# Performance work log

Hardware: AMD Instinct MI355X
Metric: run time of the kernel (lower is better)

Reference implementation:

```python
import jax, jax.numpy as jnp
import numpy as np

D = 1024
H = 8
HD = D // H
SCALE = HD ** -0.5


def setup_inputs() -> dict:
    key = jax.random.key(0)
    ks = jax.random.split(key, 12)
    s = 0.02
    return {
        "x": jax.random.normal(ks[0], (4, 2048, D), dtype=jnp.float32),
        "attn_mask": jax.random.randint(ks[1], (2048, 2048), 0, 2, dtype=jnp.int32),
        "qkv_w": jax.random.normal(ks[2], (3 * D, D), dtype=jnp.float32) * s,
        "qkv_b": jnp.zeros((3 * D,), dtype=jnp.float32),
        "q_w": jax.random.normal(ks[3], (D, D), dtype=jnp.float32) * s,
        "q_b": jnp.zeros((D,), dtype=jnp.float32),
        "k_w": jax.random.normal(ks[4], (D, D), dtype=jnp.float32) * s,
        "k_b": jnp.zeros((D,), dtype=jnp.float32),
        "v_w": jax.random.normal(ks[5], (D, D), dtype=jnp.float32) * s,
        "v_b": jnp.zeros((D,), dtype=jnp.float32),
        "out_w": jax.random.normal(ks[6], (D, D), dtype=jnp.float32) * s,
        "out_b": jnp.zeros((D,), dtype=jnp.float32),
    }


def reference(x, attn_mask, qkv_w, qkv_b, q_w, q_b, k_w, k_b, v_w, v_b, out_w, out_b):
    B, S, _ = x.shape
    qkv = x @ qkv_w.T + qkv_b
    q, k, v = jnp.split(qkv, 3, axis=-1)
    # per-stream multi-head projections, then split heads: [B,H,S,HD]
    def heads(t, w, b):
        return (t @ w.T + b).reshape(B, S, H, HD).transpose(0, 2, 1, 3)
    q = heads(q, q_w, q_b)
    k = heads(k, k_w, k_b)
    v = heads(v, v_w, v_b)
    # scaled dot-product attention with masked softmax
    scores = jnp.einsum("bhqd,bhkd->bhqk", q, k) * SCALE
    scores = jnp.where(attn_mask == 1, -jnp.inf, scores)
    attn = jax.nn.softmax(scores, axis=-1)
    o = jnp.einsum("bhqk,bhkd->bhqd", attn, v)
    o = o.transpose(0, 2, 1, 3).reshape(B, S, D)
    return o @ out_w.T + out_b
```

## Files before the change

### kernel.cpp

```cpp
#include <hip/hip_runtime.h>
#include <stdint.h>

typedef unsigned short u16;
typedef unsigned int u32;
typedef unsigned long long u64;
using f32x4 = __attribute__((ext_vector_type(4))) float;
using f32x16 = __attribute__((ext_vector_type(16))) float;
using s16x8 = __attribute__((ext_vector_type(8))) short;
using u16x4 = __attribute__((ext_vector_type(4))) unsigned short;
using u32x4 = __attribute__((ext_vector_type(4))) u32;

static constexpr float kQScale = (float)(0.08838834764831845 * 1.4426950408889634);

__device__ __forceinline__ u16 f2bf(float f) {
  uint32_t u = __float_as_uint(f);
  u += 0x7fffu + ((u >> 16) & 1u);
  return (u16)(u >> 16);
}

__device__ __forceinline__ float fexp2(float x) {
#if __has_builtin(__builtin_amdgcn_exp2f)
  return __builtin_amdgcn_exp2f(x);
#else
  return exp2f(x);
#endif
}

__device__ __forceinline__ u32 cvtpk(float lo, float hi) {
  u32 r;
  asm("v_cvt_pk_bf16_f32 %0, %1, %2" : "=v"(r) : "v"(lo), "v"(hi));
  return r;
}

__device__ __forceinline__ void mfma16(f32x4& d, s16x8 a, s16x8 b) {
  asm volatile("v_mfma_f32_16x16x32_bf16 %0, %1, %2, %0" : "+v"(d) : "v"(a), "v"(b));
}
__device__ __forceinline__ void mfma32(f32x16& d, s16x8 a, s16x8 b) {
  asm volatile("v_mfma_f32_32x32x16_bf16 %0, %1, %2, %0" : "+v"(d) : "v"(a), "v"(b));
}
__device__ __forceinline__ f32x16 mfma32_z(s16x8 a, s16x8 b) {
  f32x16 d;
  asm volatile("v_mfma_f32_32x32x16_bf16 %0, %1, %2, 0" : "=&v"(d) : "v"(a), "v"(b));
  return d;
}

__device__ __forceinline__ void g2lds16(const void* g, void* l) {
  __builtin_amdgcn_global_load_lds(
      (__attribute__((address_space(1))) void*)(uintptr_t)g,
      (__attribute__((address_space(3))) void*)(uint32_t)(uintptr_t)l, 16, 0, 0);
}

#define BAR() asm volatile("s_barrier" ::: "memory")

__global__ __launch_bounds__(256) void cvt_f32_bf16(const float* __restrict__ in,
                                                    u16* __restrict__ out, int n) {
  int i = (blockIdx.x * 256 + threadIdx.x) * 4;
  if (i + 3 < n) {
    f32x4 v = *(const f32x4*)(in + i);
    u16x4 o = {f2bf(v.x), f2bf(v.y), f2bf(v.z), f2bf(v.w)};
    *(u16x4*)(out + i) = o;
  }
}

__global__ __launch_bounds__(256) void cvt4(const float* __restrict__ a, const float* __restrict__ b,
                                            const float* __restrict__ c, const float* __restrict__ d,
                                            u16* __restrict__ out) {
  int z = blockIdx.y;
  const float* in = z == 0 ? a : z == 1 ? b : z == 2 ? c : d;
  int i = (blockIdx.x * 256 + threadIdx.x) * 4;
  f32x4 v = *(const f32x4*)(in + i);
  u16x4 o = {f2bf(v.x), f2bf(v.y), f2bf(v.z), f2bf(v.w)};
  *(u16x4*)(out + (size_t)z * 1048576 + i) = o;
}

__global__ __launch_bounds__(256) void transpose_f32_bf16(const float* __restrict__ in,
                                                          u16* __restrict__ out, int R, int C) {
  __shared__ u16 tile[32][33];
  int bx = blockIdx.x, by = blockIdx.y;
  int tx = threadIdx.x & 31, ty = threadIdx.x >> 5;
#pragma unroll
  for (int k = 0; k < 4; ++k)
    tile[ty + k * 8][tx] = f2bf(in[(size_t)(by * 32 + ty + k * 8) * C + bx * 32 + tx]);
  __syncthreads();
#pragma unroll
  for (int k = 0; k < 4; ++k)
    out[(size_t)(bx * 32 + ty + k * 8) * R + by * 32 + tx] = tile[tx][ty + k * 8];
}

__global__ __launch_bounds__(256) void cbias3(const float* __restrict__ qw, const float* __restrict__ kw,
                                              const float* __restrict__ vw, const float* __restrict__ qkvb,
                                              const float* __restrict__ qb, const float* __restrict__ kb,
                                              const float* __restrict__ vb, float* __restrict__ out) {
  int z = blockIdx.y;
  const float* w = z == 0 ? qw : (z == 1 ? kw : vw);
  const float* ba = z == 0 ? qb : (z == 1 ? kb : vb);
  const float* bi = qkvb + z * 1024;
  int o = blockIdx.x * 4 + (threadIdx.x >> 6);
  int lane = threadIdx.x & 63;
  float s = 0.f;
  for (int m = lane; m < 1024; m += 64) s += w[o * 1024 + m] * bi[m];
#pragma unroll
  for (int d = 1; d < 64; d <<= 1) s += __shfl_xor(s, d);
  if (lane == 0) {
    float fin = s + ba[o];
    if (z == 0) fin *= kQScale;
    out[z * 1024 + o] = fin;
  }
}

__global__ __launch_bounds__(256) void pack_mask(const int* __restrict__ m, u64* __restrict__ pm) {
  int row = blockIdx.x;
  int wv = threadIdx.x >> 6, lane = threadIdx.x & 63;
#pragma unroll
  for (int i = 0; i < 8; ++i) {
    int word = wv * 8 + i;
    u64 b = __ballot(m[(size_t)row * 2048 + word * 64 + lane] == 0);
    if (lane == 0) pm[(size_t)row * 32 + word] = b;
  }
}

template <typename OUT_T, bool BIAS_PER_ROW>
__global__ __launch_bounds__(256, 2) void gemm_nt(const u16* __restrict__ A, int lda, long bsA,
                                                  const u16* __restrict__ B, int ldb, long bsB,
                                                  OUT_T* __restrict__ C, int ldc, long bsC,
                                                  const float* __restrict__ bias, long bsBias,
                                                  int NtilesN, int K, float scale_z0) {
  __shared__ __align__(16) u16 As[128 * 64];
  __shared__ __align__(16) u16 Bs[128 * 64];
  const int z = blockIdx.z;
  const float sc = (z == 0) ? scale_z0 : 1.f;
  A += (size_t)z * bsA; B += (size_t)z * bsB; C += (size_t)z * bsC;
  if (bias) bias += (size_t)z * bsBias;
  const int tm = blockIdx.x / NtilesN, tn = blockIdx.x % NtilesN;
  const int tid = threadIdx.x, lane = tid & 63, w = tid >> 6;
  const int wm = w >> 1, wn = w & 1;
  const int q = lane & 15, g = lane >> 4;
  f32x4 acc[4][4] = {};

  const u16* Ab = A + (size_t)(tm * 128 + (tid >> 3)) * lda + ((tid & 7) << 3);
  const u16* Bb = B + (size_t)(tn * 128 + (tid >> 3)) * ldb + ((tid & 7) << 3);
  char* AsW = (char*)As + (w << 10);
  char* BsW = (char*)Bs + (w << 10);

  for (int k0 = 0; k0 < K; k0 += 64) {
#pragma unroll
    for (int it = 0; it < 4; ++it) {
      g2lds16(Ab + (size_t)(it * 32) * lda + k0, AsW + it * 4096);
      g2lds16(Bb + (size_t)(it * 32) * ldb + k0, BsW + it * 4096);
    }
    __syncthreads();
#pragma unroll
    for (int kk = 0; kk < 2; ++kk) {
      s16x8 af[4], bf[4];
#pragma unroll
      for (int i = 0; i < 4; ++i)
        af[i] = *(const s16x8*)((const char*)As + (wm * 64 + i * 16 + q) * 128 + kk * 64 + g * 16);
#pragma unroll
      for (int i = 0; i < 4; ++i)
        bf[i] = *(const s16x8*)((const char*)Bs + (wn * 64 + i * 16 + q) * 128 + kk * 64 + g * 16);
#pragma unroll
      for (int mf = 0; mf < 4; ++mf)
#pragma unroll
        for (int nf = 0; nf < 4; ++nf) mfma16(acc[mf][nf], af[mf], bf[nf]);
    }
    __syncthreads();
  }
  asm volatile("s_nop 7\n\ts_nop 7");
#pragma unroll
  for (int mf = 0; mf < 4; ++mf)
#pragma unroll
    for (int nf = 0; nf < 4; ++nf) {
      const int row = tm * 128 + wm * 64 + mf * 16 + g * 4;
      const int col = tn * 128 + wn * 64 + nf * 16 + q;
      float bc = (!BIAS_PER_ROW && bias) ? bias[col] : 0.f;
#pragma unroll
      for (int r = 0; r < 4; ++r) {
        float v = acc[mf][nf][r] * sc;
        if (bias) v += BIAS_PER_ROW ? bias[row + r] : bc;
        if constexpr (sizeof(OUT_T) == 2)
          C[(size_t)(row + r) * ldc + col] = (OUT_T)f2bf(v);
        else
          C[(size_t)(row + r) * ldc + col] = (OUT_T)v;
      }
    }
}

__global__ __launch_bounds__(512, 1) void gemm256(const u16* __restrict__ A, int lda,
                                                  const u16* __restrict__ B, int ldb,
                                                  u16* __restrict__ C, int ldc,
                                                  const float* __restrict__ bias,
                                                  int K, int NtN) {
  __shared__ __align__(16) u16 Als[2][256 * 64];
  __shared__ __align__(16) u16 Bls[2][256 * 64];
  const int bid = blockIdx.x;
  const int cpx = gridDim.x >> 3;
  const int wgid = (bid & 7) * cpx + (bid >> 3);
  const int tm = wgid / NtN, tn = wgid % NtN;
  const int tid = threadIdx.x, lane = tid & 63, w = tid >> 6;
  const int wm = w >> 2, wn = w & 3;
  const int q = lane & 15, g = lane >> 4, qk = q & 7;
  const int nT = K >> 6;

  f32x4 acc[8][4] = {};
  s16x8 af[4][2], bf[4][2];

  const int srow = tid >> 3, sch = tid & 7;
  const int gcol = (sch ^ (srow & 7)) << 3;
  const u16* Abase = A + (size_t)(tm * 256 + srow) * lda + gcol;
  const u16* Bbase = B + (size_t)(tn * 256 + srow) * ldb + gcol;

  auto stageA = [&](int buf, int kt, int h) {
    const u16* s0 = Abase + (size_t)(h * 128) * lda + (kt << 6);
    char* d = (char*)&Als[buf][0] + h * 16384 + (w << 10);
    g2lds16(s0, d);
    g2lds16(s0 + (size_t)64 * lda, d + 8192);
  };
  auto stageB = [&](int buf, int kt, int h) {
    const u16* s0 = Bbase + (size_t)(h * 128) * ldb + (kt << 6);
    char* d = (char*)&Bls[buf][0] + h * 16384 + (w << 10);
    g2lds16(s0, d);
    g2lds16(s0 + (size_t)64 * ldb, d + 8192);
  };
  auto loadA = [&](const char* base, int mh) {
#pragma unroll
    for (int mf = 0; mf < 4; ++mf)
#pragma unroll
      for (int kk = 0; kk < 2; ++kk)
        af[mf][kk] = *(const s16x8*)(base + (mh * 128 + wm * 64 + mf * 16 + q) * 128 +
                                     ((((kk << 2) + g) ^ qk) << 4));
  };
  auto loadB = [&](const char* base, int nh) {
#pragma unroll
    for (int nf = 0; nf < 2; ++nf)
#pragma unroll
      for (int kk = 0; kk < 2; ++kk)
        bf[nh * 2 + nf][kk] = *(const s16x8*)(base + (nh * 128 + wn * 32 + nf * 16 + q) * 128 +
                                              ((((kk << 2) + g) ^ qk) << 4));
  };
  auto quad = [&](int mh, int nh) {
    __builtin_amdgcn_s_setprio(1);
#pragma unroll
    for (int mf = 0; mf < 4; ++mf)
#pragma unroll
      for (int nf = 0; nf < 2; ++nf)
#pragma unroll
        for (int kk = 0; kk < 2; ++kk)
          mfma16(acc[mh * 4 + mf][nh * 2 + nf], af[mf][kk], bf[nh * 2 + nf][kk]);
    __builtin_amdgcn_s_setprio(0);
  };

  stageA(0, 0, 0); stageA(0, 0, 1); stageB(0, 0, 0); stageB(0, 0, 1);
  const int kt1 = (1 < nT) ? 1 : 0;
  stageB(1, kt1, 0); stageB(1, kt1, 1);
  asm volatile("s_waitcnt vmcnt(4)" ::: "memory");
  BAR();

  for (int kt = 0; kt < nT; ++kt) {
    const int buf = kt & 1;
    const char* Ab = (const char*)&Als[buf][0];
    const char* Bb = (const char*)&Bls[buf][0];
    const int ktA = (kt + 1 < nT) ? kt + 1 : nT - 1;
    const int ktB = (kt + 2 < nT) ? kt + 2 : nT - 1;
    loadA(Ab, 0); loadB(Bb, 0);
    stageA(buf ^ 1, ktA, 0);
    BAR();
    quad(0, 0);
    BAR();
    loadB(Bb, 1);
    stageA(buf ^ 1, ktA, 1);
    BAR();
    quad(0, 1);
    asm volatile("s_waitcnt vmcnt(8)" ::: "memory");
    BAR();
    loadA(Ab, 1);
    stageB(buf, ktB, 0);
    BAR();
    quad(1, 0);
    BAR();
    stageB(buf, ktB, 1);
    BAR();
    quad(1, 1);
    asm volatile("s_waitcnt vmcnt(6)" ::: "memory");
    BAR();
  }

  asm volatile("s_nop 7\n\ts_nop 7");
#pragma unroll
  for (int mf = 0; mf < 8; ++mf) {
    const int row = tm * 256 + (mf >> 2) * 128 + wm * 64 + (mf & 3) * 16 + g * 4;
#pragma unroll
    for (int nf = 0; nf < 4; ++nf) {
      const int col = tn * 256 + (nf >> 1) * 128 + wn * 32 + (nf & 1) * 16 + q;
      const float bc = bias[col];
#pragma unroll
      for (int r = 0; r < 4; ++r)
        C[(size_t)(row + r) * ldc + col] = f2bf(acc[mf][nf][r] + bc);
    }
  }
}

__global__ __launch_bounds__(256, 2) void attn_fwd(const u16* __restrict__ Qb, const u16* __restrict__ Kb,
                                                   int ldq, const u16* __restrict__ Vt,
                                                   const u64* __restrict__ pmask,
                                                   u16* __restrict__ Ob) {
  __shared__ __align__(16) char K_lds[2 * 16384];
  __shared__ __align__(16) char V_lds[2 * 16384];
  const int n = blockIdx.x;
  const int slot = n >> 3;
  const int grp = (n & 7) * 4 + (slot >> 4);
  const int qt = slot & 15;
  const int h = grp & 7, b = grp >> 3;
  const int tid = threadIdx.x, w = tid >> 6, lane = tid & 63;
  const int ql = lane & 31;
  const int hi = lane >> 5;
  const int q0 = qt * 128;

  s16x8 qf[8];
  const u16* qrow = Qb + (size_t)(b * 2048 + q0 + w * 32 + ql) * ldq + h * 128 + 8 * hi;
#pragma unroll
  for (int kd = 0; kd < 8; ++kd) qf[kd] = *(const s16x8*)(qrow + 16 * kd);

  u32x4 ov = {0x3F803F80u, 0x3F803F80u, 0x3F803F80u, 0x3F803F80u};
  const s16x8 ones = __builtin_bit_cast(s16x8, ov);

  f32x16 oacc[4] = {};
  f32x16 lacc = {};

  const int ksr = tid >> 4, ksc = tid & 15;
  const int vsr = tid >> 3, vsc = tid & 7;
  const int sw = ql & 15;

  auto stageKV = [&](int buf, int s2) {
    const int kv0 = s2 * 64;
    char* kb = K_lds + buf * 16384 + (w << 10);
    char* vb = V_lds + buf * 16384 + (w << 10);
#pragma unroll
    for (int it = 0; it < 4; ++it) {
      int kr = it * 16 + ksr;
      g2lds16(Kb + (size_t)(b * 2048 + kv0 + kr) * ldq + h * 128 + ((ksc ^ (kr & 15)) << 3),
              kb + it * 4096);
      int vr = it * 32 + vsr;
      g2lds16(Vt + (size_t)(h * 128 + vr) * 8192 + b * 2048 + kv0 + ((vsc ^ (vr & 7)) << 3),
              vb + it * 4096);
    }
  };

  stageKV(0, 0);
  __syncthreads();

  for (int s = 0; s < 32; ++s) {
    const int cur = s & 1;
    if (s + 1 < 32) stageKV(cur ^ 1, s + 1);
    const char* Kc = K_lds + cur * 16384;
    const char* Vc = V_lds + cur * 16384;

    u64 pw = pmask[(size_t)(q0 + w * 32 + ql) * 32 + s];

    f32x16 sacc0, sacc1;
    __builtin_amdgcn_s_setprio(1);
#pragma unroll
    for (int kd = 0; kd < 8; ++kd) {
      int c = (2 * kd + hi) ^ sw;
      s16x8 kf0 = *(const s16x8*)(Kc + ql * 256 + (c << 4));
      s16x8 kf1 = *(const s16x8*)(Kc + (32 + ql) * 256 + (c << 4));
      if (kd == 0) { sacc0 = mfma32_z(kf0, qf[0]); sacc1 = mfma32_z(kf1, qf[0]); }
      else         { mfma32(sacc0, kf0, qf[kd]);   mfma32(sacc1, kf1, qf[kd]); }
    }
    __builtin_amdgcn_s_setprio(0);
    asm volatile("s_nop 7\n\ts_nop 7");

    u32 Wp[8][2];
#pragma unroll
    for (int nt = 0; nt < 2; ++nt) {
      u32 halfm = (u32)(pw >> (32 * nt + 4 * hi));
#pragma unroll
      for (int t = 0; t < 4; ++t) {
        float e[4];
#pragma unroll
        for (int j = 0; j < 4; ++j) {
          float ev = fexp2(nt == 0 ? sacc0[4 * t + j] : sacc1[4 * t + j]);
          int km;
          asm("v_bfe_i32 %0, %1, %2, 1" : "=v"(km) : "v"(halfm), "n"(8 * t + j));
          e[j] = __uint_as_float(__float_as_uint(ev) & (u32)km);
        }
        Wp[nt * 4 + t][0] = cvtpk(e[0], e[1]);
        Wp[nt * 4 + t][1] = cvtpk(e[2], e[3]);
      }
    }

    s16x8 pa[4];
#pragma unroll
    for (int ks = 0; ks < 4; ++ks) {
      u32 s0 = hi ? Wp[2 * ks][0] : Wp[2 * ks + 1][0];
      u32 s1 = hi ? Wp[2 * ks][1] : Wp[2 * ks + 1][1];
      u32 r0 = (u32)__shfl_xor((int)s0, 32);
      u32 r1 = (u32)__shfl_xor((int)s1, 32);
      u32 o0 = hi ? Wp[2 * ks + 1][0] : Wp[2 * ks][0];
      u32 o1 = hi ? Wp[2 * ks + 1][1] : Wp[2 * ks][1];
      u32x4 wv;
      wv.x = hi ? r0 : o0;
      wv.y = hi ? r1 : o1;
      wv.z = hi ? o0 : r0;
      wv.w = hi ? o1 : r1;
      pa[ks] = __builtin_bit_cast(s16x8, wv);
    }
    asm volatile("s_nop 3");

    __builtin_amdgcn_s_setprio(1);
#pragma unroll
    for (int ks = 0; ks < 4; ++ks) {
#pragma unroll
      for (int dt = 0; dt < 4; ++dt) {
        int vrow = dt * 32 + ql;
        s16x8 vf = *(const s16x8*)(Vc + vrow * 128 + ((((2 * ks + hi)) ^ (vrow & 7)) << 4));
        mfma32(oacc[dt], pa[ks], vf);
      }
      mfma32(lacc, pa[ks], ones);
    }
    __builtin_amdgcn_s_setprio(0);
    __syncthreads();
  }

  asm volatile("s_nop 7\n\ts_nop 7");
#pragma unroll
  for (int dt = 0; dt < 4; ++dt)
#pragma unroll
    for (int reg = 0; reg < 16; ++reg) {
      int qr = (reg & 3) + 8 * (reg >> 2) + 4 * hi;
      size_t trow = (size_t)(b * 2048 + q0 + w * 32 + qr);
      Ob[trow * 1024 + h * 128 + dt * 32 + ql] = f2bf(oacc[dt][reg] / lacc[reg]);
    }
}

extern "C" void kernel_launch(void* const* d_in, const int* in_sizes, int n_in,
                              void* d_out, int out_size, void* d_ws, size_t ws_size,
                              hipStream_t stream) {
  (void)in_sizes; (void)n_in; (void)out_size; (void)ws_size;
  const float* x    = (const float*)d_in[0];
  const int*   am   = (const int*)d_in[1];
  const float* qkvw = (const float*)d_in[2];
  const float* qkvb = (const float*)d_in[3];
  const float* qw   = (const float*)d_in[4];
  const float* qb   = (const float*)d_in[5];
  const float* kw   = (const float*)d_in[6];
  const float* kb   = (const float*)d_in[7];
  const float* vw   = (const float*)d_in[8];
  const float* vb   = (const float*)d_in[9];
  const float* ow   = (const float*)d_in[10];
  const float* ob   = (const float*)d_in[11];

  char* p = (char*)d_ws;
  auto take = [&](size_t n) { char* r = p; p += (n + 255) & ~(size_t)255; return r; };
  u16* xb    = (u16*)take(8192ull * 1024 * 2);
  u16* qkvwT = (u16*)take(1024ull * 3072 * 2);
  u16* wb4   = (u16*)take(4ull * 1048576 * 2);
  u16* comb3 = (u16*)take(3ull * 1048576 * 2);
  float* cb3 = (float*)take(3ull * 1024 * 4);
  u16* QK2   = (u16*)take(8192ull * 2048 * 2);
  u16* V2t   = (u16*)take(8192ull * 1024 * 2);
  u64* pm    = (u64*)take(2048ull * 32 * 8);
  u16* Obuf  = xb;

  cvt_f32_bf16<<<8192, 256, 0, stream>>>(x, xb, 8192 * 1024);
  cvt4<<<dim3(1024, 4), 256, 0, stream>>>(qw, kw, vw, ow, wb4);
  transpose_f32_bf16<<<dim3(32, 96), 256, 0, stream>>>(qkvw, qkvwT, 3072, 1024);
  cbias3<<<dim3(256, 3), 256, 0, stream>>>(qw, kw, vw, qkvb, qb, kb, vb, cb3);

  gemm_nt<u16, false><<<dim3(64, 1, 3), 256, 0, stream>>>(
      wb4, 1024, 1048576, qkvwT, 3072, 1024, comb3, 1024, 1048576, nullptr, 0, 8, 1024, kQScale);
  gemm256<<<256, 512, 0, stream>>>(xb, 1024, comb3, 1024, QK2, 2048, cb3, 1024, 8);
  gemm_nt<u16, true><<<dim3(512, 1, 1), 256, 0, stream>>>(
      comb3 + 2 * 1048576, 1024, 0, xb, 1024, 0, V2t, 8192, 0, cb3 + 2048, 0, 64, 1024, 1.f);

  pack_mask<<<2048, 256, 0, stream>>>(am, pm);
  attn_fwd<<<512, 256, 0, stream>>>(QK2, QK2 + 1024, 2048, V2t, pm, Obuf);

  gemm_nt<float, false><<<dim3(512, 1, 1), 256, 0, stream>>>(
      Obuf, 1024, 0, wb4 + 3 * 1048576, 1024, 0, (float*)d_out, 1024, 0, ob, 0, 8, 1024, 1.f);
}
```

Before: 244.8 us.

## Software-pipeline attention: overlap next-tile QK with current softmax/PV, triple-buffer V

Restructures the attention main loop so the QK^T MFMAs for tile s+1 are issued while tile s's exp/mask/PV work runs, using ping-pong score registers and a two-deep prefetch. K stays double-buffered, V becomes triple-buffered, and explicit vmcnt waits with barriers replace the plain __syncthreads. The goal is to hide MFMA and exp latency and global-to-LDS load latency behind each other. In exchange it uses more LDS (80KB per block, which may limit the two-blocks-per-CU occupancy) and more live score registers, and it redundantly restages tile 31 near the end.

Result: no change. 243.7 us (-0.5%).

```diff
diff --git a/kernel.cpp b/kernel.cpp
--- a/kernel.cpp
+++ b/kernel.cpp
@@ -303,8 +303,8 @@
                                                    int ldq, const u16* __restrict__ Vt,
                                                    const u64* __restrict__ pmask,
                                                    u16* __restrict__ Ob) {
-  __shared__ __align__(16) char K_lds[2 * 16384];
-  __shared__ __align__(16) char V_lds[2 * 16384];
+  __shared__ __align__(16) char K_lds[2][16384];
+  __shared__ __align__(16) char V_lds[3][16384];
   const int n = blockIdx.x;
   const int slot = n >> 3;
   const int grp = (n & 7) * 4 + (slot >> 4);
@@ -329,96 +329,114 @@
   const int ksr = tid >> 4, ksc = tid & 15;
   const int vsr = tid >> 3, vsc = tid & 7;
   const int sw = ql & 15;
-
-  auto stageKV = [&](int buf, int s2) {
+  const u64* pmrow = pmask + (size_t)(q0 + w * 32 + ql) * 32;
+
+  auto stageK = [&](int buf, int s2) {
     const int kv0 = s2 * 64;
-    char* kb = K_lds + buf * 16384 + (w << 10);
-    char* vb = V_lds + buf * 16384 + (w << 10);
+    char* kb = K_lds[buf] + (w << 10);
 #pragma unroll
     for (int it = 0; it < 4; ++it) {
       int kr = it * 16 + ksr;
       g2lds16(Kb + (size_t)(b * 2048 + kv0 + kr) * ldq + h * 128 + ((ksc ^ (kr & 15)) << 3),
               kb + it * 4096);
+    }
+  };
+  auto stageV = [&](int buf, int s2) {
+    const int kv0 = s2 * 64;
+    char* vb = V_lds[buf] + (w << 10);
+#pragma unroll
+    for (int it = 0; it < 4; ++it) {
       int vr = it * 32 + vsr;
       g2lds16(Vt + (size_t)(h * 128 + vr) * 8192 + b * 2048 + kv0 + ((vsc ^ (vr & 7)) << 3),
               vb + it * 4096);
     }
   };
-
-  stageKV(0, 0);
-  __syncthreads();
-
-  for (int s = 0; s < 32; ++s) {
-    const int cur = s & 1;
-    if (s + 1 < 32) stageKV(cur ^ 1, s + 1);
-    const char* Kc = K_lds + cur * 16384;
-    const char* Vc = V_lds + cur * 16384;
-
-    u64 pw = pmask[(size_t)(q0 + w * 32 + ql) * 32 + s];
-
-    f32x16 sacc0, sacc1;
-    __builtin_amdgcn_s_setprio(1);
+  auto qk = [&](f32x16& d0, f32x16& d1, int kbuf) {
+    const char* Kc = K_lds[kbuf];
 #pragma unroll
     for (int kd = 0; kd < 8; ++kd) {
       int c = (2 * kd + hi) ^ sw;
       s16x8 kf0 = *(const s16x8*)(Kc + ql * 256 + (c << 4));
       s16x8 kf1 = *(const s16x8*)(Kc + (32 + ql) * 256 + (c << 4));
-      if (kd == 0) { sacc0 = mfma32_z(kf0, qf[0]); sacc1 = mfma32_z(kf1, qf[0]); }
-      else         { mfma32(sacc0, kf0, qf[kd]);   mfma32(sacc1, kf1, qf[kd]); }
-    }
-    __builtin_amdgcn_s_setprio(0);
-    asm volatile("s_nop 7\n\ts_nop 7");
-
-    u32 Wp[8][2];
-#pragma unroll
-    for (int nt = 0; nt < 2; ++nt) {
-      u32 halfm = (u32)(pw >> (32 * nt + 4 * hi));
+      if (kd == 0) { d0 = mfma32_z(kf0, qf[0]); d1 = mfma32_z(kf1, qf[0]); }
+      else         { mfma32(d0, kf0, qf[kd]);   mfma32(d1, kf1, qf[kd]); }
+    }
+  };
+
+  auto body = [&](f32x16& c0, f32x16& c1, f32x16& n0, f32x16& n1, int s, int vbR, int vbW) {
+    u64 pw = pmrow[s];
+    const int sc2 = (s + 2 < 32) ? s + 2 : 31;
+    stageK(s & 1, sc2);
+    stageV(vbW, sc2);
+    if (s + 1 < 32) qk(n0, n1, (s + 1) & 1);
+    const char* Vc = V_lds[vbR];
+    s16x8 pa[2];
+#pragma unroll
+    for (int half = 0; half < 2; ++half) {
+      u32 halfm = (u32)(pw >> (32 * half + 4 * hi));
+      u32 Wp[4][2];
 #pragma unroll
       for (int t = 0; t < 4; ++t) {
         float e[4];
 #pragma unroll
         for (int j = 0; j < 4; ++j) {
-          float ev = fexp2(nt == 0 ? sacc0[4 * t + j] : sacc1[4 * t + j]);
+          float ev = fexp2(half == 0 ? c0[4 * t + j] : c1[4 * t + j]);
           int km;
           asm("v_bfe_i32 %0, %1, %2, 1" : "=v"(km) : "v"(halfm), "n"(8 * t + j));
           e[j] = __uint_as_float(__float_as_uint(ev) & (u32)km);
         }
-        Wp[nt * 4 + t][0] = cvtpk(e[0], e[1]);
-        Wp[nt * 4 + t][1] = cvtpk(e[2], e[3]);
+        Wp[t][0] = cvtpk(e[0], e[1]);
+        Wp[t][1] = cvtpk(e[2], e[3]);
       }
-    }
-
-    s16x8 pa[4];
-#pragma unroll
-    for (int ks = 0; ks < 4; ++ks) {
-      u32 s0 = hi ? Wp[2 * ks][0] : Wp[2 * ks + 1][0];
-      u32 s1 = hi ? Wp[2 * ks][1] : Wp[2 * ks + 1][1];
-      u32 r0 = (u32)__shfl_xor((int)s0, 32);
-      u32 r1 = (u32)__shfl_xor((int)s1, 32);
-      u32 o0 = hi ? Wp[2 * ks + 1][0] : Wp[2 * ks][0];
-      u32 o1 = hi ? Wp[2 * ks + 1][1] : Wp[2 * ks][1];
-      u32x4 wv;
-      wv.x = hi ? r0 : o0;
-      wv.y = hi ? r1 : o1;
-      wv.z = hi ? o0 : r0;
-      wv.w = hi ? o1 : r1;
-      pa[ks] = __builtin_bit_cast(s16x8, wv);
-    }
-    asm volatile("s_nop 3");
-
-    __builtin_amdgcn_s_setprio(1);
-#pragma unroll
-    for (int ks = 0; ks < 4; ++ks) {
-#pragma unroll
-      for (int dt = 0; dt < 4; ++dt) {
-        int vrow = dt * 32 + ql;
-        s16x8 vf = *(const s16x8*)(Vc + vrow * 128 + ((((2 * ks + hi)) ^ (vrow & 7)) << 4));
-        mfma32(oacc[dt], pa[ks], vf);
+#pragma unroll
+      for (int kq = 0; kq < 2; ++kq) {
+        u32 s0 = hi ? Wp[2 * kq][0] : Wp[2 * kq + 1][0];
+        u32 s1 = hi ? Wp[2 * kq][1] : Wp[2 * kq + 1][1];
+        u32 r0 = (u32)__shfl_xor((int)s0, 32);
+        u32 r1 = (u32)__shfl_xor((int)s1, 32);
+        u32 o0 = hi ? Wp[2 * kq + 1][0] : Wp[2 * kq][0];
+        u32 o1 = hi ? Wp[2 * kq + 1][1] : Wp[2 * kq][1];
+        u32x4 wv;
+        wv.x = hi ? r0 : o0;
+        wv.y = hi ? r1 : o1;
+        wv.z = hi ? o0 : r0;
+        wv.w = hi ? o1 : r1;
+        pa[kq] = __builtin_bit_cast(s16x8, wv);
       }
-      mfma32(lacc, pa[ks], ones);
-    }
-    __builtin_amdgcn_s_setprio(0);
-    __syncthreads();
+      asm volatile("s_nop 3");
+      __builtin_amdgcn_s_setprio(1);
+#pragma unroll
+      for (int kq = 0; kq < 2; ++kq) {
+        const int ks = 2 * half + kq;
+#pragma unroll
+        for (int dt = 0; dt < 4; ++dt) {
+          int vrow = dt * 32 + ql;
+          s16x8 vf = *(const s16x8*)(Vc + vrow * 128 + (((2 * ks + hi) ^ (vrow & 7)) << 4));
+          mfma32(oacc[dt], pa[kq], vf);
+        }
+        mfma32(lacc, pa[kq], ones);
+      }
+      __builtin_amdgcn_s_setprio(0);
+    }
+    asm volatile("s_waitcnt vmcnt(4)" ::: "memory");
+    BAR();
+  };
+
+  stageK(0, 0); stageV(0, 0); stageK(1, 1); stageV(1, 1);
+  asm volatile("s_waitcnt vmcnt(4)" ::: "memory");
+  BAR();
+  f32x16 sA0, sA1, sB0, sB1;
+  qk(sA0, sA1, 0);
+  BAR();
+
+  int vb = 0;
+  for (int s2 = 0; s2 < 16; ++s2) {
+    const int s = 2 * s2;
+    const int vb1 = (vb + 1 == 3) ? 0 : vb + 1;
+    const int vb2 = (vb + 2 >= 3) ? vb - 1 : vb + 2;
+    body(sA0, sA1, sB0, sB1, s, vb, vb2);
+    body(sB0, sB1, sA0, sA1, s + 1, vb1, vb);
+    vb = vb2;
   }
 
   asm volatile("s_nop 7\n\ts_nop 7");
```
